# Performance work log

Measured on AMD Instinct MI355X. Metric: run time of the kernel, lower is better.

The kernel has to match this reference:

```python
import jax, jax.numpy as jnp
import numpy as np

B, S, D_IN, D_OUT = 4, 4096, 2048, 2048


def setup_inputs() -> dict:
    key = jax.random.key(0)
    kx, kw = jax.random.split(key)
    x = jax.random.normal(kx, (B, S, D_IN), dtype=jnp.float32)
    weight = jax.random.normal(kw, (D_OUT, D_IN), dtype=jnp.float32) * 0.02
    return {"x": x, "weight": weight}


def reference(x, weight):
    # Per-row absmax int8 activation quantization
    x_scale = jnp.clip(jnp.max(jnp.abs(x), axis=-1, keepdims=True), 1e-05, None)  # [B,S,1]
    x_quant = jnp.clip(jnp.round(x / x_scale * 127.0), -128.0, 127.0)
    # Ternary weight quantization (mean-centered absmean scale)
    w_mean = jnp.mean(weight)
    w_centered = weight - w_mean
    w_scale = jnp.clip(jnp.mean(jnp.abs(w_centered)), 1e-05, None)
    w_quant = jnp.clip(jnp.round(w_centered / w_scale), -1.0, 1.0)
    # GEMM on quantized values, then dequant rescale
    y = jnp.einsum('bsi,oi->bso', x_quant, w_quant)  # [B,S,D_OUT]
    y = y * (w_scale * x_scale / 127.0)
    return y.astype(x.dtype)
```

## Files before the change

### kernel.cpp

```cpp
#include <hip/hip_runtime.h>
#include <stdint.h>

#define M_TOT 16384
#define K_DIM 2048
#define N_DIM 2048
#define W_ELEMS (N_DIM * K_DIM)

typedef int v4i __attribute__((ext_vector_type(4)));

__device__ __forceinline__ void async_load16(const void* gptr, void* lptr) {
    __builtin_amdgcn_global_load_lds(
        (__attribute__((address_space(1))) void*)(uintptr_t)gptr,
        (__attribute__((address_space(3))) void*)(uint32_t)(uintptr_t)lptr,
        16, 0, 0);
}

__global__ void wsum_kernel(const float* __restrict__ w, double* __restrict__ sums) {
    int tid = blockIdx.x * 256 + threadIdx.x;
    const float4* w4 = (const float4*)w;
    double s = 0.0;
    for (int i = tid; i < W_ELEMS / 4; i += 512 * 256) {
        float4 v = w4[i];
        s += (double)v.x + (double)v.y + (double)v.z + (double)v.w;
    }
    #pragma unroll
    for (int off = 32; off; off >>= 1) s += __shfl_down(s, off);
    __shared__ double ls[4];
    if ((threadIdx.x & 63) == 0) ls[threadIdx.x >> 6] = s;
    __syncthreads();
    if (threadIdx.x == 0) atomicAdd(&sums[0], ls[0] + ls[1] + ls[2] + ls[3]);
}

__global__ void wabs_kernel(const float* __restrict__ w, double* __restrict__ sums) {
    double mean = sums[0] * (1.0 / (double)W_ELEMS);
    int tid = blockIdx.x * 256 + threadIdx.x;
    const float4* w4 = (const float4*)w;
    double s = 0.0;
    for (int i = tid; i < W_ELEMS / 4; i += 512 * 256) {
        float4 v = w4[i];
        s += fabs((double)v.x - mean) + fabs((double)v.y - mean) +
             fabs((double)v.z - mean) + fabs((double)v.w - mean);
    }
    #pragma unroll
    for (int off = 32; off; off >>= 1) s += __shfl_down(s, off);
    __shared__ double ls[4];
    if ((threadIdx.x & 63) == 0) ls[threadIdx.x >> 6] = s;
    __syncthreads();
    if (threadIdx.x == 0) atomicAdd(&sums[1], ls[0] + ls[1] + ls[2] + ls[3]);
}

__device__ __forceinline__ int qclamp(float v, int lo, int hi) {
    int q = (int)rintf(v);
    q = q > hi ? hi : (q < lo ? lo : q);
    return q & 255;
}

__global__ void wquant_kernel(const float* __restrict__ w, const double* __restrict__ sums,
                              int8_t* __restrict__ wq) {
    float mean  = (float)(sums[0] * (1.0 / (double)W_ELEMS));
    float scale = (float)fmax(sums[1] * (1.0 / (double)W_ELEMS), 1e-5);
    int i = blockIdx.x * 256 + threadIdx.x;
    float4 v = ((const float4*)w)[i];
    int p = qclamp((v.x - mean) / scale, -1, 1)
          | (qclamp((v.y - mean) / scale, -1, 1) << 8)
          | (qclamp((v.z - mean) / scale, -1, 1) << 16)
          | (qclamp((v.w - mean) / scale, -1, 1) << 24);
    ((int*)wq)[i] = p;
}

__global__ void xquant_kernel(const float* __restrict__ x, int8_t* __restrict__ xq,
                              float* __restrict__ xscale) {
    int row = blockIdx.x;
    int t = threadIdx.x;
    const float4* xr = (const float4*)(x + (size_t)row * K_DIM);
    float4 v0 = xr[t];
    float4 v1 = xr[t + 256];
    float m = fmaxf(fmaxf(fmaxf(fabsf(v0.x), fabsf(v0.y)), fmaxf(fabsf(v0.z), fabsf(v0.w))),
                    fmaxf(fmaxf(fabsf(v1.x), fabsf(v1.y)), fmaxf(fabsf(v1.z), fabsf(v1.w))));
    #pragma unroll
    for (int off = 32; off; off >>= 1) m = fmaxf(m, __shfl_down(m, off));
    __shared__ float ls[4];
    if ((t & 63) == 0) ls[t >> 6] = m;
    __syncthreads();
    float scale = fmaxf(fmaxf(fmaxf(ls[0], ls[1]), fmaxf(ls[2], ls[3])), 1e-5f);
    if (t == 0) xscale[row] = scale;
    int* outp = (int*)(xq + (size_t)row * K_DIM);
    int p0 = qclamp(v0.x / scale * 127.0f, -128, 127)
           | (qclamp(v0.y / scale * 127.0f, -128, 127) << 8)
           | (qclamp(v0.z / scale * 127.0f, -128, 127) << 16)
           | (qclamp(v0.w / scale * 127.0f, -128, 127) << 24);
    int p1 = qclamp(v1.x / scale * 127.0f, -128, 127)
           | (qclamp(v1.y / scale * 127.0f, -128, 127) << 8)
           | (qclamp(v1.z / scale * 127.0f, -128, 127) << 16)
           | (qclamp(v1.w / scale * 127.0f, -128, 127) << 24);
    outp[t]       = p0;
    outp[t + 256] = p1;
}

__global__ __launch_bounds__(256) void gemm_i8_kernel(
    const int8_t* __restrict__ xq, const int8_t* __restrict__ wq,
    const float* __restrict__ xscale, const double* __restrict__ sums,
    float* __restrict__ out)
{
    __shared__ __align__(16) int8_t lsA[2][128 * 64];
    __shared__ __align__(16) int8_t lsB[2][128 * 64];
    const int tid  = threadIdx.x;
    const int lane = tid & 63;
    const int wv   = tid >> 6;
    const int bn = blockIdx.x, bm = blockIdx.y;

    const int8_t* gA = xq + (size_t)bm * 128 * K_DIM;
    const int8_t* gB = wq + (size_t)bn * 128 * K_DIM;

    const int r = tid >> 2;
    const int s = tid & 3;
    const int c = s ^ ((r >> 1) & 3);
    const size_t gOff0 = (size_t)r * K_DIM + c * 16;
    const size_t gOff1 = gOff0 + (size_t)64 * K_DIM;

    v4i acc[4][4] = {};

    const int wm = (wv >> 1) * 64;
    const int wn = (wv & 1) * 64;
    const int fc = lane >> 4;
    const int fr = lane & 15;

    int aoff[4], boff[4];
    #pragma unroll
    for (int i = 0; i < 4; i++) {
        int ra = wm + i * 16 + fr;
        aoff[i] = ra * 64 + (fc ^ ((ra >> 1) & 3)) * 16;
        int rb = wn + i * 16 + fr;
        boff[i] = rb * 64 + (fc ^ ((rb >> 1) & 3)) * 16;
    }

    #define STAGE(buf, k0)                                            \
        do {                                                          \
            async_load16(gA + gOff0 + (k0), lsA[buf] + tid * 16);     \
            async_load16(gA + gOff1 + (k0), lsA[buf] + 4096 + tid * 16); \
            async_load16(gB + gOff0 + (k0), lsB[buf] + tid * 16);     \
            async_load16(gB + gOff1 + (k0), lsB[buf] + 4096 + tid * 16); \
        } while (0)

    #define COMPUTE(buf)                                              \
        do {                                                          \
            v4i af[4], bf[4];                                         \
            _Pragma("unroll")                                         \
            for (int i = 0; i < 4; i++) af[i] = *(const v4i*)(lsA[buf] + aoff[i]); \
            _Pragma("unroll")                                         \
            for (int i = 0; i < 4; i++) bf[i] = *(const v4i*)(lsB[buf] + boff[i]); \
            _Pragma("unroll")                                         \
            for (int mi = 0; mi < 4; mi++)                            \
                _Pragma("unroll")                                     \
                for (int nj = 0; nj < 4; nj++)                        \
                    acc[mi][nj] = __builtin_amdgcn_mfma_i32_16x16x64_i8( \
                        af[mi], bf[nj], acc[mi][nj], 0, 0, 0);        \
        } while (0)

    STAGE(0, 0);
    for (int k0 = 0; k0 < K_DIM; k0 += 128) {
        __syncthreads();
        if (k0 + 64 < K_DIM) STAGE(1, k0 + 64);
        COMPUTE(0);
        __syncthreads();
        if (k0 + 128 < K_DIM) STAGE(0, k0 + 128);
        COMPUTE(1);
    }
    #undef STAGE
    #undef COMPUTE

    float wscale = (float)fmax(sums[1] * (1.0 / (double)W_ELEMS), 1e-5);
    float f127 = wscale * (1.0f / 127.0f);
    #pragma unroll
    for (int mi = 0; mi < 4; mi++) {
        #pragma unroll
        for (int rg = 0; rg < 4; rg++) {
            int mg = bm * 128 + wm + mi * 16 + (lane >> 4) * 4 + rg;
            float fs = f127 * xscale[mg];
            float* orow = out + (size_t)mg * N_DIM + bn * 128 + wn;
            #pragma unroll
            for (int nj = 0; nj < 4; nj++)
                orow[nj * 16 + fr] = fs * (float)acc[mi][nj][rg];
        }
    }
}

extern "C" void kernel_launch(void* const* d_in, const int* in_sizes, int n_in,
                              void* d_out, int out_size, void* d_ws, size_t ws_size,
                              hipStream_t stream) {
    const float* x = (const float*)d_in[0];
    const float* w = (const float*)d_in[1];
    float* out = (float*)d_out;

    char* ws = (char*)d_ws;
    double* sums   = (double*)ws;
    float*  xscale = (float*)(ws + 64);
    int8_t* xq     = (int8_t*)(ws + 64 + 65536);
    int8_t* wq     = (int8_t*)(ws + 64 + 65536 + (size_t)M_TOT * K_DIM);

    hipMemsetAsync(sums, 0, 16, stream);
    wsum_kernel <<<512, 256, 0, stream>>>(w, sums);
    wabs_kernel <<<512, 256, 0, stream>>>(w, sums);
    wquant_kernel<<<W_ELEMS / 1024, 256, 0, stream>>>(w, sums, wq);
    xquant_kernel<<<M_TOT, 256, 0, stream>>>(x, xq, xscale);
    gemm_i8_kernel<<<dim3(N_DIM / 128, M_TOT / 128), 256, 0, stream>>>(xq, wq, xscale, sums, out);
}
```

Before: 334.7 us.

## Use 256x256 GEMM tiles with 8 waves, phased pipelining, and wave-per-row xquant

The int8 GEMM moves from 128x128 tiles with 4 waves to 256x256 tiles with 8 waves, each wave computing a 128x64 sub-tile. It splits every K step into four phases, overlapping async global-to-LDS loads with MFMA work through explicit vmcnt waits, raw barriers and setprio. Block IDs are remapped for locality. The activation quantizer now handles one row per wave with shuffle-xor reductions, which removes the shared-memory sync. The changes aim to raise arithmetic intensity and cut load stalls, at the cost of 128KB of LDS per block, more accumulator registers and fragile manual synchronisation.

```diff
diff --git a/kernel.cpp b/kernel.cpp
--- a/kernel.cpp
+++ b/kernel.cpp
@@ -68,116 +68,149 @@
     ((int*)wq)[i] = p;
 }
 
-__global__ void xquant_kernel(const float* __restrict__ x, int8_t* __restrict__ xq,
-                              float* __restrict__ xscale) {
-    int row = blockIdx.x;
-    int t = threadIdx.x;
+__global__ __launch_bounds__(256) void xquant_kernel(const float* __restrict__ x,
+                                                     int8_t* __restrict__ xq,
+                                                     float* __restrict__ xscale) {
+    const int row  = (blockIdx.x << 2) | (threadIdx.x >> 6);
+    const int lane = threadIdx.x & 63;
     const float4* xr = (const float4*)(x + (size_t)row * K_DIM);
-    float4 v0 = xr[t];
-    float4 v1 = xr[t + 256];
-    float m = fmaxf(fmaxf(fmaxf(fabsf(v0.x), fabsf(v0.y)), fmaxf(fabsf(v0.z), fabsf(v0.w))),
-                    fmaxf(fmaxf(fabsf(v1.x), fabsf(v1.y)), fmaxf(fabsf(v1.z), fabsf(v1.w))));
-    #pragma unroll
-    for (int off = 32; off; off >>= 1) m = fmaxf(m, __shfl_down(m, off));
-    __shared__ float ls[4];
-    if ((t & 63) == 0) ls[t >> 6] = m;
-    __syncthreads();
-    float scale = fmaxf(fmaxf(fmaxf(ls[0], ls[1]), fmaxf(ls[2], ls[3])), 1e-5f);
-    if (t == 0) xscale[row] = scale;
+    float4 v[8];
+    #pragma unroll
+    for (int i = 0; i < 8; i++) v[i] = xr[lane + (i << 6)];
+    float m = 0.0f;
+    #pragma unroll
+    for (int i = 0; i < 8; i++) {
+        m = fmaxf(m, fmaxf(fmaxf(fabsf(v[i].x), fabsf(v[i].y)),
+                           fmaxf(fabsf(v[i].z), fabsf(v[i].w))));
+    }
+    #pragma unroll
+    for (int off = 32; off; off >>= 1) m = fmaxf(m, __shfl_xor(m, off));
+    const float scale = fmaxf(m, 1e-5f);
+    if (lane == 0) xscale[row] = scale;
     int* outp = (int*)(xq + (size_t)row * K_DIM);
-    int p0 = qclamp(v0.x / scale * 127.0f, -128, 127)
-           | (qclamp(v0.y / scale * 127.0f, -128, 127) << 8)
-           | (qclamp(v0.z / scale * 127.0f, -128, 127) << 16)
-           | (qclamp(v0.w / scale * 127.0f, -128, 127) << 24);
-    int p1 = qclamp(v1.x / scale * 127.0f, -128, 127)
-           | (qclamp(v1.y / scale * 127.0f, -128, 127) << 8)
-           | (qclamp(v1.z / scale * 127.0f, -128, 127) << 16)
-           | (qclamp(v1.w / scale * 127.0f, -128, 127) << 24);
-    outp[t]       = p0;
-    outp[t + 256] = p1;
-}
-
-__global__ __launch_bounds__(256) void gemm_i8_kernel(
+    #pragma unroll
+    for (int i = 0; i < 8; i++) {
+        int p = qclamp(v[i].x / scale * 127.0f, -128, 127)
+              | (qclamp(v[i].y / scale * 127.0f, -128, 127) << 8)
+              | (qclamp(v[i].z / scale * 127.0f, -128, 127) << 16)
+              | (qclamp(v[i].w / scale * 127.0f, -128, 127) << 24);
+        outp[lane + (i << 6)] = p;
+    }
+}
+
+__global__ __launch_bounds__(512, 2) void gemm_i8_kernel(
     const int8_t* __restrict__ xq, const int8_t* __restrict__ wq,
     const float* __restrict__ xscale, const double* __restrict__ sums,
     float* __restrict__ out)
 {
-    __shared__ __align__(16) int8_t lsA[2][128 * 64];
-    __shared__ __align__(16) int8_t lsB[2][128 * 64];
+    __shared__ __align__(16) int8_t lsA[2][32768];
+    __shared__ __align__(16) int8_t lsB[2][32768];
+
     const int tid  = threadIdx.x;
     const int lane = tid & 63;
     const int wv   = tid >> 6;
-    const int bn = blockIdx.x, bm = blockIdx.y;
-
-    const int8_t* gA = xq + (size_t)bm * 128 * K_DIM;
-    const int8_t* gB = wq + (size_t)bn * 128 * K_DIM;
-
-    const int r = tid >> 2;
-    const int s = tid & 3;
-    const int c = s ^ ((r >> 1) & 3);
-    const size_t gOff0 = (size_t)r * K_DIM + c * 16;
-    const size_t gOff1 = gOff0 + (size_t)64 * K_DIM;
-
-    v4i acc[4][4] = {};
-
-    const int wm = (wv >> 1) * 64;
-    const int wn = (wv & 1) * 64;
-    const int fc = lane >> 4;
-    const int fr = lane & 15;
-
-    int aoff[4], boff[4];
-    #pragma unroll
-    for (int i = 0; i < 4; i++) {
+
+    const int flat = blockIdx.x;
+    const int nf   = ((flat & 7) << 6) | (flat >> 3);
+    const int bm   = nf >> 3;
+    const int bn   = nf & 7;
+
+    const int sChunk = ((tid & 3) ^ ((tid >> 3) & 3)) << 4;
+    const int8_t* gAb = xq + (size_t)(bm * 256 + (tid >> 2)) * K_DIM + sChunk;
+    const int8_t* gBb = wq + (size_t)(bn * 256 + (tid >> 2)) * K_DIM + sChunk;
+    const int sDst = tid * 16;
+
+    #define STAGE(OP, NB, K0, KH)                                              \
+        do {                                                                   \
+            async_load16(g##OP##b + (K0) + (KH) * 64,                          \
+                         ls##OP[NB] + (KH) * 16384 + sDst);                    \
+            async_load16(g##OP##b + (K0) + (KH) * 64 + (size_t)128 * K_DIM,    \
+                         ls##OP[NB] + (KH) * 16384 + 8192 + sDst);             \
+        } while (0)
+
+    #define VM4 asm volatile("s_waitcnt vmcnt(4)" ::: "memory")
+    #define VM0 asm volatile("s_waitcnt vmcnt(0)" ::: "memory")
+
+    const int wm  = (wv >> 2) * 128;
+    const int wn  = (wv & 3) * 64;
+    const int fr  = lane & 15;
+    const int fcl = lane >> 4;
+    int aoff[8], boff[4];
+    #pragma unroll
+    for (int i = 0; i < 8; i++) {
         int ra = wm + i * 16 + fr;
-        aoff[i] = ra * 64 + (fc ^ ((ra >> 1) & 3)) * 16;
-        int rb = wn + i * 16 + fr;
-        boff[i] = rb * 64 + (fc ^ ((rb >> 1) & 3)) * 16;
-    }
-
-    #define STAGE(buf, k0)                                            \
-        do {                                                          \
-            async_load16(gA + gOff0 + (k0), lsA[buf] + tid * 16);     \
-            async_load16(gA + gOff1 + (k0), lsA[buf] + 4096 + tid * 16); \
-            async_load16(gB + gOff0 + (k0), lsB[buf] + tid * 16);     \
-            async_load16(gB + gOff1 + (k0), lsB[buf] + 4096 + tid * 16); \
+        aoff[i] = ra * 64 + ((fcl ^ ((ra >> 1) & 3)) << 4);
+    }
+    #pragma unroll
+    for (int j = 0; j < 4; j++) {
+        int rb = wn + j * 16 + fr;
+        boff[j] = rb * 64 + ((fcl ^ ((rb >> 1) & 3)) << 4);
+    }
+
+    v4i acc[8][4] = {};
+    v4i bf[4];
+
+    #define PHASE(CB, KH, Q, LOADB, EXTRA)                                     \
+        do {                                                                   \
+            const int8_t* pA_ = lsA[CB] + (KH) * 16384;                        \
+            const int8_t* pB_ = lsB[CB] + (KH) * 16384;                        \
+            v4i af[4];                                                         \
+            _Pragma("unroll")                                                  \
+            for (int i_ = 0; i_ < 4; i_++)                                     \
+                af[i_] = *(const v4i*)(pA_ + aoff[(Q) * 4 + i_]);              \
+            if (LOADB) {                                                       \
+                _Pragma("unroll")                                              \
+                for (int j_ = 0; j_ < 4; j_++)                                 \
+                    bf[j_] = *(const v4i*)(pB_ + boff[j_]);                    \
+            }                                                                  \
+            EXTRA;                                                             \
+            __builtin_amdgcn_s_barrier();                                      \
+            __builtin_amdgcn_s_setprio(1);                                     \
+            _Pragma("unroll")                                                  \
+            for (int i_ = 0; i_ < 4; i_++)                                     \
+                _Pragma("unroll")                                              \
+                for (int j_ = 0; j_ < 4; j_++)                                 \
+                    acc[(Q) * 4 + i_][j_] =                                    \
+                        __builtin_amdgcn_mfma_i32_16x16x64_i8(                 \
+                            af[i_], bf[j_], acc[(Q) * 4 + i_][j_], 0, 0, 0);   \
+            __builtin_amdgcn_s_setprio(0);                                     \
+            __builtin_amdgcn_s_barrier();                                      \
         } while (0)
 
-    #define COMPUTE(buf)                                              \
-        do {                                                          \
-            v4i af[4], bf[4];                                         \
-            _Pragma("unroll")                                         \
-            for (int i = 0; i < 4; i++) af[i] = *(const v4i*)(lsA[buf] + aoff[i]); \
-            _Pragma("unroll")                                         \
-            for (int i = 0; i < 4; i++) bf[i] = *(const v4i*)(lsB[buf] + boff[i]); \
-            _Pragma("unroll")                                         \
-            for (int mi = 0; mi < 4; mi++)                            \
-                _Pragma("unroll")                                     \
-                for (int nj = 0; nj < 4; nj++)                        \
-                    acc[mi][nj] = __builtin_amdgcn_mfma_i32_16x16x64_i8( \
-                        af[mi], bf[nj], acc[mi][nj], 0, 0, 0);        \
-        } while (0)
-
-    STAGE(0, 0);
-    for (int k0 = 0; k0 < K_DIM; k0 += 128) {
-        __syncthreads();
-        if (k0 + 64 < K_DIM) STAGE(1, k0 + 64);
-        COMPUTE(0);
-        __syncthreads();
-        if (k0 + 128 < K_DIM) STAGE(0, k0 + 128);
-        COMPUTE(1);
-    }
+    STAGE(A, 0, 0, 0);
+    STAGE(B, 0, 0, 0);
+    STAGE(A, 0, 0, 1);
+    STAGE(B, 0, 0, 1);
+    VM4;
+    __builtin_amdgcn_s_barrier();
+
+    for (int t = 0; t < 15; ++t) {
+        const int cur = t & 1, nxt = cur ^ 1;
+        const int kn = (t + 1) << 7;
+        PHASE(cur, 0, 0, true,  STAGE(A, nxt, kn, 0));
+        PHASE(cur, 0, 1, false, STAGE(B, nxt, kn, 0); VM4);
+        PHASE(cur, 1, 0, true,  STAGE(A, nxt, kn, 1));
+        PHASE(cur, 1, 1, false, STAGE(B, nxt, kn, 1); VM4);
+    }
+    PHASE(1, 0, 0, true,  (void)0);
+    PHASE(1, 0, 1, false, VM0);
+    PHASE(1, 1, 0, true,  (void)0);
+    PHASE(1, 1, 1, false, (void)0);
+
+    #undef PHASE
     #undef STAGE
-    #undef COMPUTE
+    #undef VM4
+    #undef VM0
 
     float wscale = (float)fmax(sums[1] * (1.0 / (double)W_ELEMS), 1e-5);
     float f127 = wscale * (1.0f / 127.0f);
     #pragma unroll
-    for (int mi = 0; mi < 4; mi++) {
+    for (int mi = 0; mi < 8; mi++) {
         #pragma unroll
         for (int rg = 0; rg < 4; rg++) {
-            int mg = bm * 128 + wm + mi * 16 + (lane >> 4) * 4 + rg;
+            int mg = bm * 256 + wm + mi * 16 + (lane >> 4) * 4 + rg;
             float fs = f127 * xscale[mg];
-            float* orow = out + (size_t)mg * N_DIM + bn * 128 + wn;
+            float* orow = out + (size_t)mg * N_DIM + bn * 256 + wn;
             #pragma unroll
             for (int nj = 0; nj < 4; nj++)
                 orow[nj * 16 + fr] = fs * (float)acc[mi][nj][rg];
@@ -202,6 +235,6 @@
     wsum_kernel <<<512, 256, 0, stream>>>(w, sums);
     wabs_kernel <<<512, 256, 0, stream>>>(w, sums);
     wquant_kernel<<<W_ELEMS / 1024, 256, 0, stream>>>(w, sums, wq);
-    xquant_kernel<<<M_TOT, 256, 0, stream>>>(x, xq, xscale);
-    gemm_i8_kernel<<<dim3(N_DIM / 128, M_TOT / 128), 256, 0, stream>>>(xq, wq, xscale, sums, out);
-}
+    xquant_kernel<<<M_TOT / 4, 256, 0, stream>>>(x, xq, xscale);
+    gemm_i8_kernel<<<dim3(N_DIM / 256 * (M_TOT / 256)), 512, 0, stream>>>(xq, wq, xscale, sums, out);
+}
```

Result: faster. 322.2 us (-3.7%).
